# Performance work log

Measured on AMD Instinct MI355X. Metric: run time of the kernel, lower is better.

## Reference

```python
import jax, jax.numpy as jnp
import numpy as np

Q, A, R, S, K = 256, 28, 512, 256, 2  # n_quantize, n_aux, n_resch, n_skipch, kernel_size
DEPTH, REPEAT = 10, 3
L = DEPTH * REPEAT  # 30 layers
T = 8192


def setup_inputs() -> dict:
    key = jax.random.key(0)
    ks = jax.random.split(key, 24)
    w = lambda k, shape: jax.random.normal(k, shape, dtype=jnp.float32) * 0.05
    return {
        "x": jax.random.randint(ks[0], (1, T), 0, Q, dtype=jnp.int32),
        "h": jax.random.normal(ks[1], (1, A, T), dtype=jnp.float32),
        "Wc": w(ks[2], (R, Q, K)), "bc": w(ks[3], (R,)),
        "Wds": w(ks[4], (L, R, R, K)), "bds": w(ks[5], (L, R)),
        "Wdt": w(ks[6], (L, R, R, K)), "bdt": w(ks[7], (L, R)),
        "Was": w(ks[8], (L, R, A, 1)), "bas": w(ks[9], (L, R)),
        "Wat": w(ks[10], (L, R, A, 1)), "bat": w(ks[11], (L, R)),
        "Wsk": w(ks[12], (L, S, R, 1)), "bsk": w(ks[13], (L, S)),
        "Wr": w(ks[14], (L, R, R, 1)), "br": w(ks[15], (L, R)),
        "Wp1": w(ks[16], (S, S, 1)), "bp1": w(ks[17], (S,)),
        "Wp2": w(ks[18], (Q, S, 1)), "bp2": w(ks[19], (Q,)),
    }


def _cconv(z, w, b, d):
    # causal dilated conv: z [1,C,T], w [O,C,K] -> [1,O,T]
    pad = (w.shape[2] - 1) * d
    y = jax.lax.conv_general_dilated(
        z, w, window_strides=(1,), padding=[(pad, 0)], rhs_dilation=(d,),
        dimension_numbers=("NCH", "OIH", "NCH"))
    return y + b[None, :, None]


def reference(x, h, Wc, bc, Wds, bds, Wdt, bdt, Was, bas, Wat, bat,
              Wsk, bsk, Wr, br, Wp1, bp1, Wp2, bp2):
    dilations = [2 ** i for i in range(DEPTH)] * REPEAT
    oh = jax.nn.one_hot(x, Q, dtype=Wc.dtype).transpose(0, 2, 1)  # [1,Q,T]
    out = _cconv(oh, Wc, bc, 1)  # [1,R,T]
    skip_sum = jnp.zeros((1, S, oh.shape[2]), dtype=Wc.dtype)
    for l, d in enumerate(dilations):
        s = _cconv(out, Wds[l], bds[l], d) + _cconv(h, Was[l], bas[l], 1)
        t = _cconv(out, Wdt[l], bdt[l], d) + _cconv(h, Wat[l], bat[l], 1)
        g = jax.nn.sigmoid(s) * jnp.tanh(t)  # gated activation
        skip_sum = skip_sum + _cconv(g, Wsk[l], bsk[l], 1)
        out = _cconv(g, Wr[l], br[l], 1) + out  # residual
    o = jax.nn.relu(skip_sum)
    o = jax.nn.relu(_cconv(o, Wp1, bp1, 1))
    o = _cconv(o, Wp2, bp2, 1)  # [1,Q,T]
    return o[0].T  # [T,Q], matches squeeze(0).transpose(0,1)
```

## Files before the change

kernel.cpp:

```cpp
#include <hip/hip_runtime.h>
#include <hip/hip_bf16.h>
#include <math.h>
#include <stdint.h>

#define T_LEN 8192
#define RCH   512
#define SCH   256
#define QCH   256
#define ACH   28
#define NLAYER 30
#define KGATE 1088
#define KSR   512
#define KPOST 256

typedef _Float16 f16x8 __attribute__((ext_vector_type(8)));
typedef float    f32x4 __attribute__((ext_vector_type(4)));

static __device__ __forceinline__ unsigned short f2h(float v) {
    _Float16 h = (_Float16)v;
    return *reinterpret_cast<unsigned short*>(&h);
}

#define G2L(SRC, DST) __builtin_amdgcn_global_load_lds(                        \
    (__attribute__((address_space(1))) void*)(const void*)(SRC),              \
    (__attribute__((address_space(3))) void*)(void*)(DST), 16, 0, 0)

__global__ void pack_gate_kernel(const float* __restrict__ Wds,
                                 const float* __restrict__ Wdt,
                                 const float* __restrict__ Was,
                                 const float* __restrict__ Wat,
                                 unsigned short* __restrict__ dst) {
    int l = blockIdx.y;
    int e = blockIdx.x * 256 + threadIdx.x;
    int tile = e >> 9;
    int r9 = e & 511;
    int lane = r9 >> 3, i = r9 & 7;
    int mt = tile / 34, kt = tile % 34;
    int m = mt * 16 + (lane & 15);
    int k = kt * 32 + (lane >> 4) * 8 + i;
    int br = m & 1, ch = m >> 1;
    const float* Wd = (br ? Wdt : Wds) + (size_t)l * RCH * RCH * 2;
    const float* Wa = (br ? Wat : Was) + (size_t)l * RCH * ACH;
    float v;
    if (k < 512)       v = Wd[((size_t)ch * 512 + k) * 2 + 0];
    else if (k < 1024) v = Wd[((size_t)ch * 512 + (k - 512)) * 2 + 1];
    else { int a = k - 1024; v = (a < ACH) ? Wa[(size_t)ch * ACH + a] : 0.f; }
    dst[(size_t)l * 1024 * KGATE + e] = f2h(v);
}

__global__ void pack_sr_kernel(const float* __restrict__ Wsk,
                               const float* __restrict__ Wr,
                               unsigned short* __restrict__ dst) {
    int l = blockIdx.y;
    int e = blockIdx.x * 256 + threadIdx.x;
    int tile = e >> 9;
    int r9 = e & 511;
    int lane = r9 >> 3, i = r9 & 7;
    int mt = tile >> 4, kt = tile & 15;
    int m = mt * 16 + (lane & 15);
    int k = kt * 32 + (lane >> 4) * 8 + i;
    float v = (m < SCH) ? Wsk[(size_t)l * SCH * RCH + (size_t)m * 512 + k]
                        : Wr[(size_t)l * RCH * RCH + (size_t)(m - SCH) * 512 + k];
    dst[(size_t)l * 768 * KSR + e] = f2h(v);
}

__global__ void pack_post_kernel(const float* __restrict__ W,
                                 unsigned short* __restrict__ dst) {
    int e = blockIdx.x * 256 + threadIdx.x;
    int tile = e >> 9;
    int r9 = e & 511;
    int lane = r9 >> 3, i = r9 & 7;
    int mt = tile >> 3, kt = tile & 7;
    int m = mt * 16 + (lane & 15);
    int k = kt * 32 + (lane >> 4) * 8 + i;
    dst[e] = f2h(W[(size_t)m * 256 + k]);
}

__global__ void embed_kernel2(const int* __restrict__ x,
                              const float* __restrict__ Wc,
                              const float* __restrict__ bc,
                              float* __restrict__ out_tm,
                              unsigned short* __restrict__ outhf) {
    int idx = blockIdx.x * 256 + threadIdx.x;
    int t = idx >> 9, r = idx & 511;
    float v = Wc[((size_t)r * QCH + x[t]) * 2 + 1] + bc[r];
    if (t > 0) v += Wc[((size_t)r * QCH + x[t - 1]) * 2 + 0];
    out_tm[idx] = v;
    outhf[(size_t)idx + 512 * 512] = f2h(v);
}

__global__ void packh_kernel(const float* __restrict__ h,
                             unsigned short* __restrict__ h_tm) {
    int idx = blockIdx.x * 256 + threadIdx.x;
    int t = idx >> 6, a = idx & 63;
    h_tm[idx] = f2h(a < ACH ? h[(size_t)a * T_LEN + t] : 0.f);
}

__global__ void reluconv_kernel(const float* __restrict__ skip,
                                unsigned short* __restrict__ dst) {
    int idx = blockIdx.x * 256 + threadIdx.x;
    dst[idx] = f2h(fmaxf(skip[idx], 0.f));
}

template<int MODE, int KT64, int MB>
__global__ __launch_bounds__(256) void mfma_gemm(
    const unsigned short* __restrict__ Apk,
    const unsigned short* __restrict__ B0,
    const unsigned short* __restrict__ B2,
    const float* __restrict__ bias0, const float* __restrict__ bias1,
    const float* __restrict__ bias2, const float* __restrict__ bias3,
    float* __restrict__ O0, float* __restrict__ O1,
    unsigned short* __restrict__ OB, int dil)
{
    constexpr int KT32 = KT64 * 2;
    constexpr int NWG = MB * 64;
    constexpr int CPX = NWG / 8;

    __shared__ unsigned short Bsm[128 * 64];

    const int tid  = threadIdx.x;
    const int lane = tid & 63, wave = tid >> 6;
    const int wm = wave & 1, wn = wave >> 1;

    const int bid = blockIdx.x;
    const int swz = (bid & 7) * CPX + (bid >> 3);
    const int mb  = swz % MB;
    const int tb  = swz / MB;
    const int m0  = mb * 128;
    const int t0  = tb * 128;

    const int kc   = ((lane & 7) ^ (lane >> 3)) * 8;
    const int rsub = lane >> 3;

    f32x4 acc[4][4];
    #pragma unroll
    for (int a = 0; a < 4; ++a)
        #pragma unroll
        for (int b = 0; b < 4; ++b) acc[a][b] = (f32x4){0.f, 0.f, 0.f, 0.f};

    const size_t mt0 = (size_t)(mb * 8) + wm * 4;

    for (int kt = 0; kt < KT64; ++kt) {
        const int kb = kt * 64;
        #pragma unroll
        for (int j = 0; j < 4; ++j) {
            const int row = wave * 32 + j * 8 + rsub;
            const int tg  = t0 + row;
            const unsigned short* src;
            if constexpr (MODE == 0) {
                if (kb < 512)
                    src = B0 + (size_t)(512 + tg - dil) * 512 + kb + kc;
                else if (kb < 1024)
                    src = B0 + (size_t)(512 + tg) * 512 + (kb - 512) + kc;
                else
                    src = B2 + (size_t)tg * 64 + kc;
            } else if constexpr (MODE == 1) {
                src = B0 + (size_t)tg * 512 + kb + kc;
            } else {
                src = B0 + (size_t)tg * 256 + kb + kc;
            }
            G2L(src, &Bsm[(wave * 4 + j) * 512]);
        }

        f16x8 afr[4][2];
        #pragma unroll
        for (int mi = 0; mi < 4; ++mi)
            #pragma unroll
            for (int ks = 0; ks < 2; ++ks)
                afr[mi][ks] = *(const f16x8*)(Apk +
                    ((mt0 + mi) * KT32 + (size_t)(kt * 2 + ks)) * 512 + lane * 8);

        __syncthreads();

        f16x8 bfr[4][2];
        #pragma unroll
        for (int ni = 0; ni < 4; ++ni)
            #pragma unroll
            for (int ks = 0; ks < 2; ++ks) {
                const int trow = wn * 64 + ni * 16 + (lane & 15);
                const int kch  = ks * 4 + (lane >> 4);
                const int sch  = kch ^ (lane & 7);
                bfr[ni][ks] = *(const f16x8*)&Bsm[trow * 64 + sch * 8];
            }

        #pragma unroll
        for (int mi = 0; mi < 4; ++mi)
            #pragma unroll
            for (int ni = 0; ni < 4; ++ni) {
                acc[mi][ni] = __builtin_amdgcn_mfma_f32_16x16x32_f16(
                    afr[mi][0], bfr[ni][0], acc[mi][ni], 0, 0, 0);
                acc[mi][ni] = __builtin_amdgcn_mfma_f32_16x16x32_f16(
                    afr[mi][1], bfr[ni][1], acc[mi][ni], 0, 0, 0);
            }

        __syncthreads();
    }

    const int rb0 = (lane >> 4) * 4;
    #pragma unroll
    for (int mi = 0; mi < 4; ++mi) {
        #pragma unroll
        for (int ni = 0; ni < 4; ++ni) {
            int m = m0 + wm * 64 + mi * 16 + rb0;
            int t = t0 + wn * 64 + ni * 16 + (lane & 15);
            f32x4 v = acc[mi][ni];
            if constexpr (MODE == 0) {
                int c0 = m >> 1;
                float s0 = v.x + bias0[c0]     + bias2[c0];
                float tv0 = v.y + bias1[c0]     + bias3[c0];
                float s1 = v.z + bias0[c0 + 1] + bias2[c0 + 1];
                float tv1 = v.w + bias1[c0 + 1] + bias3[c0 + 1];
                float g0 = (1.f / (1.f + __expf(-s0))) * tanhf(tv0);
                float g1 = (1.f / (1.f + __expf(-s1))) * tanhf(tv1);
                unsigned int p = (unsigned int)f2h(g0) | ((unsigned int)f2h(g1) << 16);
                *(unsigned int*)&OB[(size_t)t * 512 + c0] = p;
            } else if constexpr (MODE == 1) {
                if (m < SCH) {
                    float4* p = (float4*)&O0[(size_t)t * 256 + m];
                    float4 o = *p;
                    o.x += v.x + bias0[m + 0];
                    o.y += v.y + bias0[m + 1];
                    o.z += v.z + bias0[m + 2];
                    o.w += v.w + bias0[m + 3];
                    *p = o;
                } else {
                    int c = m - SCH;
                    float4* p = (float4*)&O1[(size_t)t * 512 + c];
                    float4 o = *p;
                    o.x += v.x + bias1[c + 0];
                    o.y += v.y + bias1[c + 1];
                    o.z += v.z + bias1[c + 2];
                    o.w += v.w + bias1[c + 3];
                    *p = o;
                    uint2 pk;
                    pk.x = (unsigned int)f2h(o.x) | ((unsigned int)f2h(o.y) << 16);
                    pk.y = (unsigned int)f2h(o.z) | ((unsigned int)f2h(o.w) << 16);
                    *(uint2*)&OB[(size_t)(512 + t) * 512 + c] = pk;
                }
            } else if constexpr (MODE == 2) {
                float o0 = fmaxf(v.x + bias0[m + 0], 0.f);
                float o1 = fmaxf(v.y + bias0[m + 1], 0.f);
                float o2 = fmaxf(v.z + bias0[m + 2], 0.f);
                float o3 = fmaxf(v.w + bias0[m + 3], 0.f);
                uint2 pk;
                pk.x = (unsigned int)f2h(o0) | ((unsigned int)f2h(o1) << 16);
                pk.y = (unsigned int)f2h(o2) | ((unsigned int)f2h(o3) << 16);
                *(uint2*)&OB[(size_t)t * 256 + m] = pk;
            } else {
                float4 o;
                o.x = v.x + bias0[m + 0];
                o.y = v.y + bias0[m + 1];
                o.z = v.z + bias0[m + 2];
                o.w = v.w + bias0[m + 3];
                *(float4*)&O0[(size_t)t * 256 + m] = o;
            }
        }
    }
}

extern "C" void kernel_launch(void* const* d_in, const int* in_sizes, int n_in,
                              void* d_out, int out_size, void* d_ws, size_t ws_size,
                              hipStream_t stream) {
    const int*   x   = (const int*)  d_in[0];
    const float* h   = (const float*)d_in[1];
    const float* Wc  = (const float*)d_in[2];
    const float* bc  = (const float*)d_in[3];
    const float* Wds = (const float*)d_in[4];
    const float* bds = (const float*)d_in[5];
    const float* Wdt = (const float*)d_in[6];
    const float* bdt = (const float*)d_in[7];
    const float* Was = (const float*)d_in[8];
    const float* bas = (const float*)d_in[9];
    const float* Wat = (const float*)d_in[10];
    const float* bat = (const float*)d_in[11];
    const float* Wsk = (const float*)d_in[12];
    const float* bsk = (const float*)d_in[13];
    const float* Wr  = (const float*)d_in[14];
    const float* br  = (const float*)d_in[15];
    const float* Wp1 = (const float*)d_in[16];
    const float* bp1 = (const float*)d_in[17];
    const float* Wp2 = (const float*)d_in[18];
    const float* bp2 = (const float*)d_in[19];
    float* dout = (float*)d_out;

    const size_t WG_EL  = (size_t)1024 * KGATE;
    const size_t WSR_EL = (size_t)768 * KSR;
    char* w = (char*)d_ws;
    float*          out_tm = (float*)w;               w += (size_t)T_LEN * 512 * 4;
    unsigned short* outhf  = (unsigned short*)w;      w += (size_t)(T_LEN + 512) * 512 * 2;
    unsigned short* g_tm   = (unsigned short*)w;      w += (size_t)T_LEN * 512 * 2;
    unsigned short* h_tm   = (unsigned short*)w;      w += (size_t)T_LEN * 64 * 2;
    unsigned short* skiphf = (unsigned short*)w;      w += (size_t)T_LEN * 256 * 2;
    unsigned short* o1hf   = (unsigned short*)w;      w += (size_t)T_LEN * 256 * 2;
    unsigned short* Wp1_pk = (unsigned short*)w;      w += (size_t)256 * 256 * 2;
    unsigned short* Wp2_pk = (unsigned short*)w;      w += (size_t)256 * 256 * 2;
    unsigned short* Wg_pk  = (unsigned short*)w;
    size_t used_base = (size_t)((char*)Wg_pk - (char*)d_ws);
    size_t need_bulk = used_base + (WG_EL + WSR_EL) * NLAYER * 2;
    const bool bulk = ws_size >= need_bulk;
    unsigned short* Wsr_pk = Wg_pk + (bulk ? WG_EL * NLAYER : WG_EL);
    float* skip = dout;

    hipMemsetAsync(skip, 0, (size_t)T_LEN * 256 * 4, stream);
    hipMemsetAsync(outhf, 0, (size_t)512 * 512 * 2, stream);

    embed_kernel2<<<(T_LEN * 512) / 256, 256, 0, stream>>>(x, Wc, bc, out_tm, outhf);
    packh_kernel<<<(T_LEN * 64) / 256, 256, 0, stream>>>(h, h_tm);
    pack_post_kernel<<<256, 256, 0, stream>>>(Wp1, Wp1_pk);
    pack_post_kernel<<<256, 256, 0, stream>>>(Wp2, Wp2_pk);

    if (bulk) {
        pack_gate_kernel<<<dim3(4352, NLAYER), 256, 0, stream>>>(Wds, Wdt, Was, Wat, Wg_pk);
        pack_sr_kernel<<<dim3(1536, NLAYER), 256, 0, stream>>>(Wsk, Wr, Wsr_pk);
    }

    for (int l = 0; l < NLAYER; ++l) {
        int dil = 1 << (l % 10);
        const unsigned short* wg;
        const unsigned short* wsr;
        if (bulk) {
            wg  = Wg_pk  + (size_t)l * WG_EL;
            wsr = Wsr_pk + (size_t)l * WSR_EL;
        } else {
            pack_gate_kernel<<<dim3(4352, 1), 256, 0, stream>>>(
                Wds + (size_t)l * RCH * RCH * 2, Wdt + (size_t)l * RCH * RCH * 2,
                Was + (size_t)l * RCH * ACH, Wat + (size_t)l * RCH * ACH, Wg_pk);
            pack_sr_kernel<<<dim3(1536, 1), 256, 0, stream>>>(
                Wsk + (size_t)l * SCH * RCH, Wr + (size_t)l * RCH * RCH, Wsr_pk);
            wg = Wg_pk; wsr = Wsr_pk;
        }
        mfma_gemm<0, KGATE / 64, 8><<<512, 256, 0, stream>>>(
            wg, outhf, h_tm,
            bds + (size_t)l * RCH, bdt + (size_t)l * RCH,
            bas + (size_t)l * RCH, bat + (size_t)l * RCH,
            nullptr, nullptr, g_tm, dil);
        mfma_gemm<1, KSR / 64, 6><<<384, 256, 0, stream>>>(
            wsr, g_tm, nullptr,
            bsk + (size_t)l * SCH, br + (size_t)l * RCH, nullptr, nullptr,
            skip, out_tm, outhf, 0);
    }

    reluconv_kernel<<<(T_LEN * 256) / 256, 256, 0, stream>>>(skip, skiphf);
    mfma_gemm<2, KPOST / 64, 2><<<128, 256, 0, stream>>>(
        Wp1_pk, skiphf, nullptr, bp1, nullptr, nullptr, nullptr,
        nullptr, nullptr, o1hf, 0);
    mfma_gemm<3, KPOST / 64, 2><<<128, 256, 0, stream>>>(
        Wp2_pk, o1hf, nullptr, bp2, nullptr, nullptr, nullptr,
        dout, nullptr, nullptr, 0);
}
```

Measured before the change: 1.711 ms.

## Double-buffer GEMM LDS tiles and vectorize weight packing and embedding kernels

The MFMA GEMM now keeps two LDS buffers for the B tile. It issues the global-to-LDS load for the next k-tile before computing on the current one, which drops one barrier per iteration and overlaps loading with MFMA work. Separately, the weight packing kernels and the relu-convert kernel now have each thread handle 8 elements, using float4 loads and 16-byte stores. The embedding first transposes Wc so each time step reads contiguous rows with vector loads. The cost is double the LDS per block, which may lower occupancy, plus one extra transpose launch and workspace buffer.

Measured after the change: 1.764 ms. 1.03x slower.

```diff
diff --git a/kernel.cpp b/kernel.cpp
--- a/kernel.cpp
+++ b/kernel.cpp
@@ -25,68 +25,115 @@
     (__attribute__((address_space(1))) void*)(const void*)(SRC),              \
     (__attribute__((address_space(3))) void*)(void*)(DST), 16, 0, 0)
 
-__global__ void pack_gate_kernel(const float* __restrict__ Wds,
-                                 const float* __restrict__ Wdt,
-                                 const float* __restrict__ Was,
-                                 const float* __restrict__ Wat,
-                                 unsigned short* __restrict__ dst) {
+__global__ void pack_gate_v(const float* __restrict__ Wds,
+                            const float* __restrict__ Wdt,
+                            const float* __restrict__ Was,
+                            const float* __restrict__ Wat,
+                            unsigned short* __restrict__ dst) {
     int l = blockIdx.y;
-    int e = blockIdx.x * 256 + threadIdx.x;
-    int tile = e >> 9;
-    int r9 = e & 511;
-    int lane = r9 >> 3, i = r9 & 7;
+    int c = blockIdx.x * 256 + threadIdx.x;
+    int tile = c >> 6, lane = c & 63;
     int mt = tile / 34, kt = tile % 34;
-    int m = mt * 16 + (lane & 15);
-    int k = kt * 32 + (lane >> 4) * 8 + i;
+    int m  = mt * 16 + (lane & 15);
+    int k0 = kt * 32 + (lane >> 4) * 8;
     int br = m & 1, ch = m >> 1;
     const float* Wd = (br ? Wdt : Wds) + (size_t)l * RCH * RCH * 2;
     const float* Wa = (br ? Wat : Was) + (size_t)l * RCH * ACH;
-    float v;
-    if (k < 512)       v = Wd[((size_t)ch * 512 + k) * 2 + 0];
-    else if (k < 1024) v = Wd[((size_t)ch * 512 + (k - 512)) * 2 + 1];
-    else { int a = k - 1024; v = (a < ACH) ? Wa[(size_t)ch * ACH + a] : 0.f; }
-    dst[(size_t)l * 1024 * KGATE + e] = f2h(v);
-}
-
-__global__ void pack_sr_kernel(const float* __restrict__ Wsk,
-                               const float* __restrict__ Wr,
-                               unsigned short* __restrict__ dst) {
+    unsigned short o[8];
+    if (k0 < 512) {
+        const float* base = Wd + ((size_t)ch * 512 + k0) * 2;
+        #pragma unroll
+        for (int q = 0; q < 4; ++q) {
+            float4 v = *(const float4*)(base + q * 4);
+            o[q * 2 + 0] = f2h(v.x);
+            o[q * 2 + 1] = f2h(v.z);
+        }
+    } else if (k0 < 1024) {
+        const float* base = Wd + ((size_t)ch * 512 + (k0 - 512)) * 2;
+        #pragma unroll
+        for (int q = 0; q < 4; ++q) {
+            float4 v = *(const float4*)(base + q * 4);
+            o[q * 2 + 0] = f2h(v.y);
+            o[q * 2 + 1] = f2h(v.w);
+        }
+    } else {
+        int a0 = k0 - 1024;
+        #pragma unroll
+        for (int i = 0; i < 8; ++i)
+            o[i] = (a0 + i < ACH) ? f2h(Wa[(size_t)ch * ACH + a0 + i]) : (unsigned short)0;
+    }
+    *(uint4*)&dst[(size_t)l * 1024 * KGATE + (size_t)tile * 512 + lane * 8] = *(uint4*)o;
+}
+
+__global__ void pack_sr_v(const float* __restrict__ Wsk,
+                          const float* __restrict__ Wr,
+                          unsigned short* __restrict__ dst) {
     int l = blockIdx.y;
-    int e = blockIdx.x * 256 + threadIdx.x;
-    int tile = e >> 9;
-    int r9 = e & 511;
-    int lane = r9 >> 3, i = r9 & 7;
+    int c = blockIdx.x * 256 + threadIdx.x;
+    int tile = c >> 6, lane = c & 63;
     int mt = tile >> 4, kt = tile & 15;
-    int m = mt * 16 + (lane & 15);
-    int k = kt * 32 + (lane >> 4) * 8 + i;
-    float v = (m < SCH) ? Wsk[(size_t)l * SCH * RCH + (size_t)m * 512 + k]
-                        : Wr[(size_t)l * RCH * RCH + (size_t)(m - SCH) * 512 + k];
-    dst[(size_t)l * 768 * KSR + e] = f2h(v);
-}
-
-__global__ void pack_post_kernel(const float* __restrict__ W,
-                                 unsigned short* __restrict__ dst) {
-    int e = blockIdx.x * 256 + threadIdx.x;
-    int tile = e >> 9;
-    int r9 = e & 511;
-    int lane = r9 >> 3, i = r9 & 7;
+    int m  = mt * 16 + (lane & 15);
+    int k0 = kt * 32 + (lane >> 4) * 8;
+    const float* row = (m < SCH) ? (Wsk + (size_t)l * SCH * RCH + (size_t)m * 512)
+                                 : (Wr  + (size_t)l * RCH * RCH + (size_t)(m - SCH) * 512);
+    float4 v0 = *(const float4*)(row + k0);
+    float4 v1 = *(const float4*)(row + k0 + 4);
+    unsigned short o[8] = { f2h(v0.x), f2h(v0.y), f2h(v0.z), f2h(v0.w),
+                            f2h(v1.x), f2h(v1.y), f2h(v1.z), f2h(v1.w) };
+    *(uint4*)&dst[(size_t)l * 768 * KSR + (size_t)tile * 512 + lane * 8] = *(uint4*)o;
+}
+
+__global__ void pack_post_v(const float* __restrict__ W,
+                            unsigned short* __restrict__ dst) {
+    int c = blockIdx.x * 256 + threadIdx.x;
+    int tile = c >> 6, lane = c & 63;
     int mt = tile >> 3, kt = tile & 7;
-    int m = mt * 16 + (lane & 15);
-    int k = kt * 32 + (lane >> 4) * 8 + i;
-    dst[e] = f2h(W[(size_t)m * 256 + k]);
-}
-
-__global__ void embed_kernel2(const int* __restrict__ x,
-                              const float* __restrict__ Wc,
-                              const float* __restrict__ bc,
-                              float* __restrict__ out_tm,
-                              unsigned short* __restrict__ outhf) {
+    int m  = mt * 16 + (lane & 15);
+    int k0 = kt * 32 + (lane >> 4) * 8;
+    float4 v0 = *(const float4*)(W + (size_t)m * 256 + k0);
+    float4 v1 = *(const float4*)(W + (size_t)m * 256 + k0 + 4);
+    unsigned short o[8] = { f2h(v0.x), f2h(v0.y), f2h(v0.z), f2h(v0.w),
+                            f2h(v1.x), f2h(v1.y), f2h(v1.z), f2h(v1.w) };
+    *(uint4*)&dst[(size_t)tile * 512 + lane * 8] = *(uint4*)o;
+}
+
+__global__ void transpose_wc(const float* __restrict__ Wc,
+                             float* __restrict__ WcT) {
     int idx = blockIdx.x * 256 + threadIdx.x;
-    int t = idx >> 9, r = idx & 511;
-    float v = Wc[((size_t)r * QCH + x[t]) * 2 + 1] + bc[r];
-    if (t > 0) v += Wc[((size_t)r * QCH + x[t - 1]) * 2 + 0];
-    out_tm[idx] = v;
-    outhf[(size_t)idx + 512 * 512] = f2h(v);
+    int r = idx >> 9;
+    int qt = idx & 511;
+    int q = qt >> 1, tap = qt & 1;
+    WcT[(size_t)q * 1024 + tap * 512 + r] = Wc[(size_t)r * 512 + qt];
+}
+
+__global__ void embed_v(const int* __restrict__ x,
+                        const float* __restrict__ WcT,
+                        const float* __restrict__ bc,
+                        float* __restrict__ out_tm,
+                        unsigned short* __restrict__ outhf) {
+    int idx = blockIdx.x * 256 + threadIdx.x;
+    int t = idx >> 6, rc = (idx & 63) * 8;
+    int x1 = x[t];
+    const float* w1 = WcT + (size_t)x1 * 1024 + 512 + rc;
+    float4 a = *(const float4*)w1;
+    float4 b = *(const float4*)(w1 + 4);
+    float4 c0 = *(const float4*)(bc + rc);
+    float4 c1 = *(const float4*)(bc + rc + 4);
+    a.x += c0.x; a.y += c0.y; a.z += c0.z; a.w += c0.w;
+    b.x += c1.x; b.y += c1.y; b.z += c1.z; b.w += c1.w;
+    if (t > 0) {
+        const float* w0 = WcT + (size_t)x[t - 1] * 1024 + rc;
+        float4 d0 = *(const float4*)w0;
+        float4 d1 = *(const float4*)(w0 + 4);
+        a.x += d0.x; a.y += d0.y; a.z += d0.z; a.w += d0.w;
+        b.x += d1.x; b.y += d1.y; b.z += d1.z; b.w += d1.w;
+    }
+    size_t o = (size_t)t * 512 + rc;
+    *(float4*)&out_tm[o] = a;
+    *(float4*)&out_tm[o + 4] = b;
+    unsigned short p[8] = { f2h(a.x), f2h(a.y), f2h(a.z), f2h(a.w),
+                            f2h(b.x), f2h(b.y), f2h(b.z), f2h(b.w) };
+    *(uint4*)&outhf[o + 512 * 512] = *(uint4*)p;
 }
 
 __global__ void packh_kernel(const float* __restrict__ h,
@@ -96,10 +143,16 @@
     h_tm[idx] = f2h(a < ACH ? h[(size_t)a * T_LEN + t] : 0.f);
 }
 
-__global__ void reluconv_kernel(const float* __restrict__ skip,
-                                unsigned short* __restrict__ dst) {
-    int idx = blockIdx.x * 256 + threadIdx.x;
-    dst[idx] = f2h(fmaxf(skip[idx], 0.f));
+__global__ void reluconv_v(const float* __restrict__ skip,
+                           unsigned short* __restrict__ dst) {
+    int idx = (blockIdx.x * 256 + threadIdx.x) * 8;
+    float4 v0 = *(const float4*)(skip + idx);
+    float4 v1 = *(const float4*)(skip + idx + 4);
+    unsigned short o[8] = { f2h(fmaxf(v0.x, 0.f)), f2h(fmaxf(v0.y, 0.f)),
+                            f2h(fmaxf(v0.z, 0.f)), f2h(fmaxf(v0.w, 0.f)),
+                            f2h(fmaxf(v1.x, 0.f)), f2h(fmaxf(v1.y, 0.f)),
+                            f2h(fmaxf(v1.z, 0.f)), f2h(fmaxf(v1.w, 0.f)) };
+    *(uint4*)&dst[idx] = *(uint4*)o;
 }
 
 template<int MODE, int KT64, int MB>
@@ -116,7 +169,7 @@
     constexpr int NWG = MB * 64;
     constexpr int CPX = NWG / 8;
 
-    __shared__ unsigned short Bsm[128 * 64];
+    __shared__ unsigned short Bsm[2][128 * 64];
 
     const int tid  = threadIdx.x;
     const int lane = tid & 63, wave = tid >> 6;
@@ -132,15 +185,7 @@
     const int kc   = ((lane & 7) ^ (lane >> 3)) * 8;
     const int rsub = lane >> 3;
 
-    f32x4 acc[4][4];
-    #pragma unroll
-    for (int a = 0; a < 4; ++a)
-        #pragma unroll
-        for (int b = 0; b < 4; ++b) acc[a][b] = (f32x4){0.f, 0.f, 0.f, 0.f};
-
-    const size_t mt0 = (size_t)(mb * 8) + wm * 4;
-
-    for (int kt = 0; kt < KT64; ++kt) {
+    auto stage_tile = [&](int kt, int buf) {
         const int kb = kt * 64;
         #pragma unroll
         for (int j = 0; j < 4; ++j) {
@@ -159,8 +204,24 @@
             } else {
                 src = B0 + (size_t)tg * 256 + kb + kc;
             }
-            G2L(src, &Bsm[(wave * 4 + j) * 512]);
+            G2L(src, &Bsm[buf][(wave * 4 + j) * 512]);
         }
+    };
+
+    f32x4 acc[4][4];
+    #pragma unroll
+    for (int a = 0; a < 4; ++a)
+        #pragma unroll
+        for (int b = 0; b < 4; ++b) acc[a][b] = (f32x4){0.f, 0.f, 0.f, 0.f};
+
+    const size_t mt0 = (size_t)(mb * 8) + wm * 4;
+
+    stage_tile(0, 0);
+    __syncthreads();
+
+    int cur = 0;
+    for (int kt = 0; kt < KT64; ++kt, cur ^= 1) {
+        if (kt + 1 < KT64) stage_tile(kt + 1, cur ^ 1);
 
         f16x8 afr[4][2];
         #pragma unroll
@@ -169,8 +230,6 @@
             for (int ks = 0; ks < 2; ++ks)
                 afr[mi][ks] = *(const f16x8*)(Apk +
                     ((mt0 + mi) * KT32 + (size_t)(kt * 2 + ks)) * 512 + lane * 8);
-
-        __syncthreads();
 
         f16x8 bfr[4][2];
         #pragma unroll
@@ -180,7 +239,7 @@
                 const int trow = wn * 64 + ni * 16 + (lane & 15);
                 const int kch  = ks * 4 + (lane >> 4);
                 const int sch  = kch ^ (lane & 7);
-                bfr[ni][ks] = *(const f16x8*)&Bsm[trow * 64 + sch * 8];
+                bfr[ni][ks] = *(const f16x8*)&Bsm[cur][trow * 64 + sch * 8];
             }
 
         #pragma unroll
@@ -294,6 +353,7 @@
     unsigned short* o1hf   = (unsigned short*)w;      w += (size_t)T_LEN * 256 * 2;
     unsigned short* Wp1_pk = (unsigned short*)w;      w += (size_t)256 * 256 * 2;
     unsigned short* Wp2_pk = (unsigned short*)w;      w += (size_t)256 * 256 * 2;
+    float*          WcT    = (float*)w;               w += (size_t)QCH * 2 * RCH * 4;
     unsigned short* Wg_pk  = (unsigned short*)w;
     size_t used_base = (size_t)((char*)Wg_pk - (char*)d_ws);
     size_t need_bulk = used_base + (WG_EL + WSR_EL) * NLAYER * 2;
@@ -304,14 +364,15 @@
     hipMemsetAsync(skip, 0, (size_t)T_LEN * 256 * 4, stream);
     hipMemsetAsync(outhf, 0, (size_t)512 * 512 * 2, stream);
 
-    embed_kernel2<<<(T_LEN * 512) / 256, 256, 0, stream>>>(x, Wc, bc, out_tm, outhf);
+    transpose_wc<<<1024, 256, 0, stream>>>(Wc, WcT);
+    embed_v<<<(T_LEN * 64) / 256, 256, 0, stream>>>(x, WcT, bc, out_tm, outhf);
     packh_kernel<<<(T_LEN * 64) / 256, 256, 0, stream>>>(h, h_tm);
-    pack_post_kernel<<<256, 256, 0, stream>>>(Wp1, Wp1_pk);
-    pack_post_kernel<<<256, 256, 0, stream>>>(Wp2, Wp2_pk);
+    pack_post_v<<<32, 256, 0, stream>>>(Wp1, Wp1_pk);
+    pack_post_v<<<32, 256, 0, stream>>>(Wp2, Wp2_pk);
 
     if (bulk) {
-        pack_gate_kernel<<<dim3(4352, NLAYER), 256, 0, stream>>>(Wds, Wdt, Was, Wat, Wg_pk);
-        pack_sr_kernel<<<dim3(1536, NLAYER), 256, 0, stream>>>(Wsk, Wr, Wsr_pk);
+        pack_gate_v<<<dim3(544, NLAYER), 256, 0, stream>>>(Wds, Wdt, Was, Wat, Wg_pk);
+        pack_sr_v<<<dim3(192, NLAYER), 256, 0, stream>>>(Wsk, Wr, Wsr_pk);
     }
 
     for (int l = 0; l < NLAYER; ++l) {
@@ -322,10 +383,10 @@
             wg  = Wg_pk  + (size_t)l * WG_EL;
             wsr = Wsr_pk + (size_t)l * WSR_EL;
         } else {
-            pack_gate_kernel<<<dim3(4352, 1), 256, 0, stream>>>(
+            pack_gate_v<<<dim3(544, 1), 256, 0, stream>>>(
                 Wds + (size_t)l * RCH * RCH * 2, Wdt + (size_t)l * RCH * RCH * 2,
                 Was + (size_t)l * RCH * ACH, Wat + (size_t)l * RCH * ACH, Wg_pk);
-            pack_sr_kernel<<<dim3(1536, 1), 256, 0, stream>>>(
+            pack_sr_v<<<dim3(192, 1), 256, 0, stream>>>(
                 Wsk + (size_t)l * SCH * RCH, Wr + (size_t)l * RCH * RCH, Wsr_pk);
             wg = Wg_pk; wsr = Wsr_pk;
         }
@@ -340,7 +401,7 @@
             skip, out_tm, outhf, 0);
     }
 
-    reluconv_kernel<<<(T_LEN * 256) / 256, 256, 0, stream>>>(skip, skiphf);
+    reluconv_v<<<(T_LEN * 256 / 8) / 256, 256, 0, stream>>>(skip, skiphf);
     mfma_gemm<2, KPOST / 64, 2><<<128, 256, 0, stream>>>(
         Wp1_pk, skiphf, nullptr, bp1, nullptr, nullptr, nullptr,
         nullptr, nullptr, o1hf, 0);
```
